# Kernel tuning notes

Measured on AMD Instinct MI355X. Metric: run time of the kernel, lower is better.

The kernel has to match this reference:

```python
import jax, jax.numpy as jnp
import numpy as np

THRESHOLD = 0.01
TOPK_RATIO = 0.7

def setup_inputs() -> dict:
    key = jax.random.key(0)
    k1, k2, k3, k4, k5 = jax.random.split(key, 5)
    B, N, F, K = 8, 2048, 512, 256
    x = jax.random.normal(k1, (B, N, F), dtype=jnp.float32)
    adj = jax.random.uniform(k2, (B, N, N), dtype=jnp.float32)
    mask = jnp.ones((B, N), dtype=jnp.float32)
    # assign_main = Linear(F->K), ReLU, Linear(K->K)
    W1 = jax.random.normal(k3, (F, K), dtype=jnp.float32) / np.sqrt(F)
    b1 = jnp.zeros((K,), dtype=jnp.float32)
    W2 = jax.random.normal(k4, (K, K), dtype=jnp.float32) / np.sqrt(K)
    b2 = jnp.zeros((K,), dtype=jnp.float32)
    return {"x": x, "adj": adj, "mask": mask, "W1": W1, "b1": b1, "W2": W2, "b2": b2}

def reference(x, adj, mask, W1, b1, W2, b2):
    B, N, Fdim = x.shape
    K = W2.shape[1]
    # soft assignment logits with masked softmax over clusters
    h = jax.nn.relu(jnp.einsum('bnf,fk->bnk', x, W1) + b1)
    logits = jnp.einsum('bnk,kl->bnl', h, W2) + b2            # [B,N,K]
    logits = logits + (-1e9) * (1.0 - mask[..., None])
    S = jax.nn.softmax(logits, axis=-1)                       # [B,N,K]
    # pooled features and pooled adjacency
    pfeat = jnp.einsum('bnk,bnf->bkf', S, x)                  # S^T x -> [B,K,F]
    mid = jnp.einsum('bnm,bmk->bnk', adj, S)                  # adj @ S
    pooled = jnp.einsum('bnk,bnl->bkl', S, mid)               # S^T adj S -> [B,K,K]
    # threshold + top-k sparsify with straight-through estimator
    topk = min(K, int(np.ceil(TOPK_RATIO * K)))
    thr_mask = (pooled >= THRESHOLD).astype(pooled.dtype)
    a_thr = pooled * thr_mask
    _, idx = jax.lax.top_k(a_thr, topk)                       # [B,K,topk]
    bi = jnp.arange(B)[:, None, None]
    ri = jnp.arange(K)[None, :, None]
    fmask = jnp.zeros_like(pooled).at[bi, ri, idx].set(1.0)
    a_sp = pooled * fmask
    a_ste = a_sp + jax.lax.stop_gradient(pooled - a_sp)       # forward == pooled
    # symmetric degree renormalization
    row_sum = a_ste.sum(axis=-1)
    d_inv_sqrt = 1.0 / jnp.sqrt(row_sum + 1e-9)
    pooled_adj = a_ste * d_inv_sqrt[:, :, None] * d_inv_sqrt[:, None, :]
    pmask = jnp.ones((B, K), dtype=x.dtype)
    return pfeat, pooled_adj, pmask
```

## Files before the change

### kernel.cpp

```cpp
#include <hip/hip_runtime.h>
#include <hip/hip_bf16.h>


typedef float f32x4 __attribute__((ext_vector_type(4)));
typedef __bf16 bf16x8 __attribute__((ext_vector_type(8)));

#define VMCNT(n) asm volatile("s_waitcnt vmcnt(" #n ")" ::: "memory")
#define LGKM0    asm volatile("s_waitcnt lgkmcnt(0)" ::: "memory")
#define SCHEDB   __builtin_amdgcn_sched_barrier(0)
#define BARRIER                                        \
  do {                                                 \
    LGKM0;                                             \
    __builtin_amdgcn_s_barrier();                      \
    asm volatile("" ::: "memory");                     \
    SCHEDB;                                            \
  } while (0)

__device__ __forceinline__ void async_load16(const void* g, void* l) {
  __builtin_amdgcn_global_load_lds((const __attribute__((address_space(1))) void*)g,
                                   (__attribute__((address_space(3))) void*)l, 16, 0, 0);
}
__device__ __forceinline__ unsigned short f2bf(float f) {
  return __builtin_bit_cast(unsigned short, (__bf16)f);
}
__device__ __forceinline__ ushort4 f4_to_bf4(float4 v) {
  ushort4 u; u.x = f2bf(v.x); u.y = f2bf(v.y); u.z = f2bf(v.z); u.w = f2bf(v.w); return u;
}

template <int ROWS, int BK, int NT>
__device__ __forceinline__ void stage_bf16(const __bf16* __restrict__ src, long long ld,
                                           __bf16* lds, int t) {
  constexpr int GR = BK / 8;
  constexpr int N = ROWS * GR / NT;
  static_assert(N >= 1, "stage too small");
#pragma unroll
  for (int c = 0; c < N; ++c) {
    const int idx = c * NT + t;
    const int row = idx / GR;
    const int g = idx % GR;
    const int gs = g ^ (row & (GR - 1) & 7);
    async_load16(src + (long long)row * ld + gs * 8, lds + idx * 8);
  }
}
template <int BK>
__device__ __forceinline__ bf16x8 frag(const __bf16* lds, int row, int kq) {
  constexpr int GR = BK / 8;
  const int g = kq ^ (row & (GR - 1) & 7);
  return *(const bf16x8*)(lds + row * BK + g * 8);
}

__global__ __launch_bounds__(256) void prep_k(const float* __restrict__ x,
                                              const float* __restrict__ W1,
                                              const float* __restrict__ W2,
                                              __bf16* __restrict__ xbT,
                                              __bf16* __restrict__ W1T,
                                              __bf16* __restrict__ W2T) {
  __shared__ float tile[64][65];
  const int tr = threadIdx.x >> 6, tc = threadIdx.x & 63;
  const int bid = blockIdx.x;
  const float* in; __bf16* out; int r0, c0, C, R;
  if (bid < 2048) {
    const int fb = bid >> 8, rest = bid & 255;
    const int nb = rest >> 3, b = rest & 7;
    in = x + (long long)b * 1048576; out = xbT + (long long)b * 1048576;
    r0 = nb * 64; c0 = fb * 64; R = 2048; C = 512;
  } else if (bid < 2080) {
    const int w = bid - 2048;
    in = W1; out = W1T; r0 = (w >> 2) * 64; c0 = (w & 3) * 64; R = 512; C = 256;
  } else {
    const int w = bid - 2080;
    in = W2; out = W2T; r0 = (w >> 2) * 64; c0 = (w & 3) * 64; R = 256; C = 256;
  }
#pragma unroll
  for (int i = 0; i < 16; ++i)
    tile[tr + i * 4][tc] = in[(long long)(r0 + tr + i * 4) * C + c0 + tc];
  __syncthreads();
#pragma unroll
  for (int i = 0; i < 16; ++i)
    out[(long long)(c0 + tr + i * 4) * R + r0 + tc] = (__bf16)tile[tc][tr + i * 4];
}

__device__ __forceinline__ void asg_compute(const __bf16* __restrict__ Abuf,
                                            const __bf16* __restrict__ Bbuf,
                                            f32x4 (&acc)[2][4], int wn, int l15, int l4) {
  bf16x8 af[2], bf[4];
#pragma unroll
  for (int i = 0; i < 2; ++i) af[i] = frag<32>(Abuf, i * 16 + l15, l4);
#pragma unroll
  for (int j = 0; j < 4; ++j) bf[j] = frag<32>(Bbuf, wn + j * 16 + l15, l4);
  __builtin_amdgcn_s_setprio(1);
#pragma unroll
  for (int i = 0; i < 2; ++i)
#pragma unroll
    for (int j = 0; j < 4; ++j)
      acc[i][j] = __builtin_amdgcn_mfma_f32_16x16x32_bf16(af[i], bf[j], acc[i][j], 0, 0, 0);
  __builtin_amdgcn_s_setprio(0);
}

__global__ __launch_bounds__(256) void assign_fused_k(
    const float* __restrict__ x, const __bf16* __restrict__ W1T,
    const __bf16* __restrict__ W2T, const float* __restrict__ b1,
    const float* __restrict__ b2, const float* __restrict__ mask,
    __bf16* __restrict__ ST) {
  __shared__ alignas(16) __bf16 Ax[2][32 * 32];
  __shared__ alignas(16) __bf16 Bw[2][256 * 32];
  __shared__ alignas(16) __bf16 hl[32 * 264];
  __shared__ float red[2][4][32];

  const int t = threadIdx.x;
  const int lane = t & 63, wave = t >> 6;
  const int l15 = lane & 15, l4 = lane >> 4;
  const int wn = wave * 64;
  const long long row0 = (long long)blockIdx.x * 32;
  const float* Xb = x + row0 * 512;

  const int arow = t >> 3, afq = t & 7;
  const int ag = afq >> 1;
  const int aoff = arow * 32 + ((ag ^ (arow & 3)) * 8) + (afq & 1) * 4;

  auto ldx = [&](int tile) -> float4 {
    return *(const float4*)(Xb + (long long)arow * 512 + tile * 32 + afq * 4);
  };
  auto sta = [&](__bf16* dst, float4 v) { *(ushort4*)&dst[aoff] = f4_to_bf4(v); };

  f32x4 acc[2][4] = {};

  float4 xA = ldx(0);
  SCHEDB;
  stage_bf16<256, 32, 256>(W1T, 512, Bw[0], t);
  SCHEDB;
  VMCNT(4); SCHEDB;
  sta(Ax[0], xA);
  float4 xB = ldx(1);
  SCHEDB;
  VMCNT(1); SCHEDB;
  BARRIER;

#pragma unroll 1
  for (int tt = 0; tt < 14; tt += 2) {
    stage_bf16<256, 32, 256>(W1T + (tt + 1) * 32, 512, Bw[1], t);
    SCHEDB;
    xA = ldx(tt + 2);
    SCHEDB;
    asg_compute(Ax[0], Bw[0], acc, wn, l15, l4);
    VMCNT(5); SCHEDB;
    sta(Ax[1], xB);
    VMCNT(1); SCHEDB;
    BARRIER;
    stage_bf16<256, 32, 256>(W1T + (tt + 2) * 32, 512, Bw[0], t);
    SCHEDB;
    xB = ldx(tt + 3);
    SCHEDB;
    asg_compute(Ax[1], Bw[1], acc, wn, l15, l4);
    VMCNT(5); SCHEDB;
    sta(Ax[0], xA);
    VMCNT(1); SCHEDB;
    BARRIER;
  }
  stage_bf16<256, 32, 256>(W1T + 15 * 32, 512, Bw[1], t);
  SCHEDB;
  asg_compute(Ax[0], Bw[0], acc, wn, l15, l4);
  VMCNT(4); SCHEDB;
  sta(Ax[1], xB);
  VMCNT(0); SCHEDB;
  BARRIER;
  asg_compute(Ax[1], Bw[1], acc, wn, l15, l4);

  stage_bf16<256, 32, 256>(W2T, 256, Bw[0], t);
  SCHEDB;
#pragma unroll
  for (int j = 0; j < 4; ++j) {
    const int col = wn + j * 16 + l15;
    const float bv = b1[col];
#pragma unroll
    for (int i = 0; i < 2; ++i)
#pragma unroll
      for (int r = 0; r < 4; ++r)
        hl[(i * 16 + l4 * 4 + r) * 264 + col] = (__bf16)fmaxf(acc[i][j][r] + bv, 0.f);
  }
  VMCNT(0); SCHEDB;
  BARRIER;

  f32x4 acc2[2][4] = {};
#pragma unroll 1
  for (int tt = 0; tt < 8; ++tt) {
    if (tt < 7) stage_bf16<256, 32, 256>(W2T + (tt + 1) * 32, 256, Bw[(tt & 1) ^ 1], t);
    SCHEDB;
    const __bf16* Bc = Bw[tt & 1];
    bf16x8 af[2], bf[4];
#pragma unroll
    for (int i = 0; i < 2; ++i)
      af[i] = *(const bf16x8*)(&hl[(i * 16 + l15) * 264 + tt * 32 + l4 * 8]);
#pragma unroll
    for (int j = 0; j < 4; ++j) bf[j] = frag<32>(Bc, wn + j * 16 + l15, l4);
#pragma unroll
    for (int i = 0; i < 2; ++i)
#pragma unroll
      for (int j = 0; j < 4; ++j)
        acc2[i][j] = __builtin_amdgcn_mfma_f32_16x16x32_bf16(af[i], bf[j], acc2[i][j], 0, 0, 0);
    VMCNT(0); SCHEDB;
    BARRIER;
  }

  float mb[2][4], mx[2][4], sm[2][4];
#pragma unroll
  for (int i = 0; i < 2; ++i)
#pragma unroll
    for (int r = 0; r < 4; ++r) {
      mb[i][r] = -1e9f * (1.0f - mask[row0 + i * 16 + l4 * 4 + r]);
      mx[i][r] = -3.4e38f;
      sm[i][r] = 0.f;
    }
#pragma unroll
  for (int j = 0; j < 4; ++j) {
    const float bv = b2[wn + j * 16 + l15];
#pragma unroll
    for (int i = 0; i < 2; ++i)
#pragma unroll
      for (int r = 0; r < 4; ++r) {
        const float v = acc2[i][j][r] + bv + mb[i][r];
        acc2[i][j][r] = v;
        mx[i][r] = fmaxf(mx[i][r], v);
      }
  }
#pragma unroll
  for (int i = 0; i < 2; ++i)
#pragma unroll
    for (int r = 0; r < 4; ++r) {
      float m = mx[i][r];
      m = fmaxf(m, __shfl_xor(m, 1, 64)); m = fmaxf(m, __shfl_xor(m, 2, 64));
      m = fmaxf(m, __shfl_xor(m, 4, 64)); m = fmaxf(m, __shfl_xor(m, 8, 64));
      mx[i][r] = m;
    }
  if (l15 == 0)
#pragma unroll
    for (int i = 0; i < 2; ++i)
#pragma unroll
      for (int r = 0; r < 4; ++r) red[0][wave][i * 16 + l4 * 4 + r] = mx[i][r];
  __syncthreads();
#pragma unroll
  for (int i = 0; i < 2; ++i)
#pragma unroll
    for (int r = 0; r < 4; ++r) {
      const int rl = i * 16 + l4 * 4 + r;
      mx[i][r] = fmaxf(fmaxf(red[0][0][rl], red[0][1][rl]),
                       fmaxf(red[0][2][rl], red[0][3][rl]));
    }
#pragma unroll
  for (int j = 0; j < 4; ++j)
#pragma unroll
    for (int i = 0; i < 2; ++i)
#pragma unroll
      for (int r = 0; r < 4; ++r) {
        const float e = __expf(acc2[i][j][r] - mx[i][r]);
        acc2[i][j][r] = e;
        sm[i][r] += e;
      }
#pragma unroll
  for (int i = 0; i < 2; ++i)
#pragma unroll
    for (int r = 0; r < 4; ++r) {
      float s = sm[i][r];
      s += __shfl_xor(s, 1, 64); s += __shfl_xor(s, 2, 64);
      s += __shfl_xor(s, 4, 64); s += __shfl_xor(s, 8, 64);
      sm[i][r] = s;
    }
  if (l15 == 0)
#pragma unroll
    for (int i = 0; i < 2; ++i)
#pragma unroll
      for (int r = 0; r < 4; ++r) red[1][wave][i * 16 + l4 * 4 + r] = sm[i][r];
  __syncthreads();
  float inv[2][4];
#pragma unroll
  for (int i = 0; i < 2; ++i)
#pragma unroll
    for (int r = 0; r < 4; ++r) {
      const int rl = i * 16 + l4 * 4 + r;
      inv[i][r] = 1.0f / (red[1][0][rl] + red[1][1][rl] + red[1][2][rl] + red[1][3][rl]);
    }
  const long long bb = row0 >> 11;
  const long long n0 = row0 & 2047;
  __bf16* Sb = ST + bb * 524288;
#pragma unroll
  for (int j = 0; j < 4; ++j) {
    const int col = wn + j * 16 + l15;
#pragma unroll
    for (int i = 0; i < 2; ++i) {
      ushort4 u;
      u.x = f2bf(acc2[i][j][0] * inv[i][0]);
      u.y = f2bf(acc2[i][j][1] * inv[i][1]);
      u.z = f2bf(acc2[i][j][2] * inv[i][2]);
      u.w = f2bf(acc2[i][j][3] * inv[i][3]);
      *(ushort4*)(Sb + (long long)col * 2048 + n0 + i * 16 + l4 * 4) = u;
    }
  }
}

__device__ __forceinline__ void adj_cmp(const __bf16* __restrict__ Abuf,
                                        const bf16x8* __restrict__ bq,
                                        f32x4 (&acc)[2][4], int l15, int l4) {
#pragma unroll
  for (int ks = 0; ks < 2; ++ks) {
    bf16x8 af[2];
#pragma unroll
    for (int i = 0; i < 2; ++i) af[i] = frag<64>(Abuf, i * 16 + l15, ks * 4 + l4);
    __builtin_amdgcn_s_setprio(1);
#pragma unroll
    for (int i = 0; i < 2; ++i)
#pragma unroll
      for (int j = 0; j < 4; ++j)
        acc[i][j] =
            __builtin_amdgcn_mfma_f32_16x16x32_bf16(af[i], bq[j * 2 + ks], acc[i][j], 0, 0, 0);
    __builtin_amdgcn_s_setprio(0);
  }
}

__global__ __launch_bounds__(256) void gemm_adj_k(const float* __restrict__ adj,
                                                  const __bf16* __restrict__ ST,
                                                  __bf16* __restrict__ midT) {
  __shared__ alignas(16) __bf16 Aa[2][32 * 64];
  const int t = threadIdx.x;
  const int lane = t & 63, wave = t >> 6;
  const int l15 = lane & 15, l4 = lane >> 4;
  const int wn = wave * 64;
  const int id = blockIdx.x;
  const int bz = id & 7;
  const long long r0 = (long long)(id >> 3) * 32;
  const float* Ab = adj + (long long)bz * 4194304 + r0 * 2048;
  const __bf16* Bb = ST + (long long)bz * 524288;

  const int arow = t >> 4, afq = t & 15;
  const int ag = afq >> 1;
  const int aoff0 = arow * 64 + ((ag ^ (arow & 7)) * 8) + (afq & 1) * 4;
  const int aoff1 = (arow + 16) * 64 + ((ag ^ ((arow + 16) & 7)) * 8) + (afq & 1) * 4;

  auto lda4 = [&](int tile, int half) -> float4 {
    return *(const float4*)(Ab + (long long)(arow + half * 16) * 2048 + tile * 64 + afq * 4);
  };
  auto sta = [&](__bf16* dst, float4 v0, float4 v1) {
    *(ushort4*)&dst[aoff0] = f4_to_bf4(v0);
    *(ushort4*)&dst[aoff1] = f4_to_bf4(v1);
  };
  auto ldb = [&](bf16x8* dst, int tile) {
#pragma unroll
    for (int j = 0; j < 4; ++j)
#pragma unroll
      for (int ks = 0; ks < 2; ++ks)
        dst[j * 2 + ks] = *(const bf16x8*)(Bb + (long long)(wn + j * 16 + l15) * 2048 +
                                           tile * 64 + ks * 32 + l4 * 8);
  };

  f32x4 acc[2][4] = {};
  bf16x8 b0[8], b1[8];

  float4 aA0 = lda4(0, 0), aA1 = lda4(0, 1);
  SCHEDB;
  ldb(b0, 0);
  SCHEDB;
  float4 aB0 = lda4(1, 0), aB1 = lda4(1, 1);
  SCHEDB;
  VMCNT(10); SCHEDB;
  sta(Aa[0], aA0, aA1);
  BARRIER;
  VMCNT(2); SCHEDB;

#pragma unroll 1
  for (int tt = 0; tt < 30; tt += 2) {
    ldb(b1, tt + 1);
    SCHEDB;
    aA0 = lda4(tt + 2, 0); aA1 = lda4(tt + 2, 1);
    SCHEDB;
    adj_cmp(Aa[0], b0, acc, l15, l4);
    VMCNT(10); SCHEDB;
    sta(Aa[1], aB0, aB1);
    BARRIER;
    VMCNT(2); SCHEDB;
    ldb(b0, tt + 2);
    SCHEDB;
    aB0 = lda4(tt + 3, 0); aB1 = lda4(tt + 3, 1);
    SCHEDB;
    adj_cmp(Aa[1], b1, acc, l15, l4);
    VMCNT(10); SCHEDB;
    sta(Aa[0], aA0, aA1);
    BARRIER;
    VMCNT(2); SCHEDB;
  }
  ldb(b1, 31);
  SCHEDB;
  adj_cmp(Aa[0], b0, acc, l15, l4);
  VMCNT(8); SCHEDB;
  sta(Aa[1], aB0, aB1);
  BARRIER;
  VMCNT(0); SCHEDB;
  adj_cmp(Aa[1], b1, acc, l15, l4);

  __bf16* Cb = midT + (long long)bz * 524288;
#pragma unroll
  for (int j = 0; j < 4; ++j) {
    const int l = wn + j * 16 + l15;
#pragma unroll
    for (int i = 0; i < 2; ++i) {
      ushort4 u;
      u.x = f2bf(acc[i][j][0]); u.y = f2bf(acc[i][j][1]);
      u.z = f2bf(acc[i][j][2]); u.w = f2bf(acc[i][j][3]);
      *(ushort4*)(Cb + (long long)l * 2048 + r0 + i * 16 + l4 * 4) = u;
    }
  }
}

__global__ __launch_bounds__(256) void gemm_feat_k(const __bf16* __restrict__ ST,
                                                   const __bf16* __restrict__ xbT,
                                                   float* __restrict__ pfeat) {
  __shared__ alignas(16) __bf16 As[3][32 * 64];
  __shared__ alignas(16) __bf16 Bs[3][64 * 64];
  const int t = threadIdx.x;
  const int lane = t & 63, wave = t >> 6;
  const int l15 = lane & 15, l4 = lane >> 4;
  const int wn = wave * 16;
  const int id = blockIdx.x;
  const int b = id & 7, j7 = id >> 3;
  const int kblk = j7 & 7, fblk = j7 >> 3;
  const __bf16* Ab = ST + (long long)b * 524288 + (long long)kblk * 32 * 2048;
  const __bf16* Bb = xbT + (long long)b * 1048576 + (long long)fblk * 64 * 2048;

  auto stage = [&](int s, int buf) {
    stage_bf16<32, 64, 256>(Ab + s * 64, 2048, (__bf16*)As + buf * 2048, t);
    stage_bf16<64, 64, 256>(Bb + s * 64, 2048, (__bf16*)Bs + buf * 4096, t);
  };
  auto cmp = [&](int buf, f32x4 (&acc)[2]) {
    const __bf16* Ac = (const __bf16*)As + buf * 2048;
    const __bf16* Bc = (const __bf16*)Bs + buf * 4096;
#pragma unroll
    for (int ks = 0; ks < 2; ++ks) {
      bf16x8 af[2], bf;
#pragma unroll
      for (int i = 0; i < 2; ++i) af[i] = frag<64>(Ac, i * 16 + l15, ks * 4 + l4);
      bf = frag<64>(Bc, wn + l15, ks * 4 + l4);
#pragma unroll
      for (int i = 0; i < 2; ++i)
        acc[i] = __builtin_amdgcn_mfma_f32_16x16x32_bf16(af[i], bf, acc[i], 0, 0, 0);
    }
  };

  f32x4 acc[2] = {};
  stage(0, 0);
  SCHEDB;
  stage(1, 1);
  SCHEDB;
  VMCNT(3); SCHEDB;
  BARRIER;

  int cur = 0, stg = 2;
#pragma unroll 1
  for (int tt = 0; tt < 30; ++tt) {
    stage(tt + 2, stg);
    SCHEDB;
    cmp(cur, acc);
    VMCNT(3); SCHEDB;
    BARRIER;
    cur = (cur == 2) ? 0 : cur + 1;
    stg = (stg == 2) ? 0 : stg + 1;
  }
  cmp(cur, acc);
  VMCNT(0); SCHEDB;
  BARRIER;
  cur = (cur == 2) ? 0 : cur + 1;
  cmp(cur, acc);

  float* out = pfeat + (long long)b * 131072;
#pragma unroll
  for (int i = 0; i < 2; ++i)
#pragma unroll
    for (int r = 0; r < 4; ++r)
      out[(long long)(kblk * 32 + i * 16 + l4 * 4 + r) * 512 + fblk * 64 + wn + l15] =
          acc[i][r];
}

__global__ __launch_bounds__(256) void gemm_pool_k(const __bf16* __restrict__ ST,
                                                   const __bf16* __restrict__ midT,
                                                   float* __restrict__ pooled) {
  __shared__ alignas(16) __bf16 As[3][32 * 64];
  __shared__ alignas(16) __bf16 Bs[3][32 * 64];
  const int t = threadIdx.x;
  const int lane = t & 63, wave = t >> 6;
  const int l15 = lane & 15, l4 = lane >> 4;
  const int wm = (wave >> 1) * 16, wn = (wave & 1) * 16;
  const int id = blockIdx.x;
  const int b = id & 7, j7 = id >> 3;
  const int kblk = j7 & 7, lblk = j7 >> 3;
  const __bf16* Ab = ST + (long long)b * 524288 + (long long)kblk * 32 * 2048;
  const __bf16* Bb = midT + (long long)b * 524288 + (long long)lblk * 32 * 2048;

  auto stage = [&](int s, int buf) {
    stage_bf16<32, 64, 256>(Ab + s * 64, 2048, (__bf16*)As + buf * 2048, t);
    stage_bf16<32, 64, 256>(Bb + s * 64, 2048, (__bf16*)Bs + buf * 2048, t);
  };
  auto cmp = [&](int buf, f32x4& acc) {
    const __bf16* Ac = (const __bf16*)As + buf * 2048;
    const __bf16* Bc = (const __bf16*)Bs + buf * 2048;
#pragma unroll
    for (int ks = 0; ks < 2; ++ks) {
      bf16x8 af = frag<64>(Ac, wm + l15, ks * 4 + l4);
      bf16x8 bf = frag<64>(Bc, wn + l15, ks * 4 + l4);
      acc = __builtin_amdgcn_mfma_f32_16x16x32_bf16(af, bf, acc, 0, 0, 0);
    }
  };

  f32x4 acc = {};
  stage(0, 0);
  SCHEDB;
  stage(1, 1);
  SCHEDB;
  VMCNT(2); SCHEDB;
  BARRIER;

  int cur = 0, stg = 2;
#pragma unroll 1
  for (int tt = 0; tt < 30; ++tt) {
    stage(tt + 2, stg);
    SCHEDB;
    cmp(cur, acc);
    VMCNT(2); SCHEDB;
    BARRIER;
    cur = (cur == 2) ? 0 : cur + 1;
    stg = (stg == 2) ? 0 : stg + 1;
  }
  cmp(cur, acc);
  VMCNT(0); SCHEDB;
  BARRIER;
  cur = (cur == 2) ? 0 : cur + 1;
  cmp(cur, acc);

  float* out = pooled + (long long)b * 65536;
#pragma unroll
  for (int r = 0; r < 4; ++r)
    out[(long long)(kblk * 32 + wm + l4 * 4 + r) * 256 + lblk * 32 + wn + l15] = acc[r];
}

__global__ __launch_bounds__(256) void rowsum_k(const float* __restrict__ pooled,
                                                float* __restrict__ dinv) {
  const int gr = blockIdx.x * 4 + (threadIdx.x >> 6);
  const int lane = threadIdx.x & 63;
  const float* p = pooled + (long long)gr * 256;
  float s = p[lane] + p[lane + 64] + p[lane + 128] + p[lane + 192];
#pragma unroll
  for (int o = 32; o > 0; o >>= 1) s += __shfl_xor(s, o, 64);
  if (lane == 0) dinv[gr] = rsqrtf(s + 1e-9f);
}

__global__ __launch_bounds__(256) void finalize_k(const float* __restrict__ pooled,
                                                  const float* __restrict__ dinv,
                                                  float* __restrict__ outAdj,
                                                  float* __restrict__ pmask) {
  const long long i = blockIdx.x * 256LL + threadIdx.x;
  const int c = (int)(i & 255);
  const int r = (int)((i >> 8) & 255);
  const int b = (int)(i >> 16);
  outAdj[i] = pooled[i] * dinv[b * 256 + r] * dinv[b * 256 + c];
  if (i < 2048) pmask[i] = 1.0f;
}

extern "C" void kernel_launch(void* const* d_in, const int* in_sizes, int n_in,
                              void* d_out, int out_size, void* d_ws, size_t ws_size,
                              hipStream_t stream) {
  (void)in_sizes; (void)n_in; (void)out_size; (void)ws_size;
  const float* x    = (const float*)d_in[0];
  const float* adj  = (const float*)d_in[1];
  const float* mask = (const float*)d_in[2];
  const float* W1   = (const float*)d_in[3];
  const float* b1   = (const float*)d_in[4];
  const float* W2   = (const float*)d_in[5];
  const float* b2   = (const float*)d_in[6];

  char* ws = (char*)d_ws;
  __bf16* ST     = (__bf16*)(ws + 0);
  __bf16* midT   = (__bf16*)(ws + 8388608);
  __bf16* xbT    = (__bf16*)(ws + 16777216);
  float*  pooled = (float*)(ws + 33554432);
  float*  dinv   = (float*)(ws + 35651584);
  __bf16* W1T    = (__bf16*)(ws + 35659776);
  __bf16* W2T    = (__bf16*)(ws + 35921920);

  float* pfeat  = (float*)d_out;
  float* outAdj = (float*)d_out + 1048576;
  float* pmask  = (float*)d_out + 1572864;

  prep_k<<<2096, 256, 0, stream>>>(x, W1, W2, xbT, W1T, W2T);
  assign_fused_k<<<512, 256, 0, stream>>>(x, W1T, W2T, b1, b2, mask, ST);
  gemm_feat_k<<<512, 256, 0, stream>>>(ST, xbT, pfeat);
  gemm_adj_k<<<512, 256, 0, stream>>>(adj, ST, midT);
  gemm_pool_k<<<512, 256, 0, stream>>>(ST, midT, pooled);
  rowsum_k<<<512, 256, 0, stream>>>(pooled, dinv);
  finalize_k<<<2048, 256, 0, stream>>>(pooled, dinv, outAdj, pmask);
}
```

Baseline: 139.8 us.

## Triple-buffer B fragments and deepen prefetch in adj@S GEMM loop

Restructures the adj @ S main loop into a 6-step unrolled pipeline that rotates three B register buffers, so B fragments are prefetched two tiles ahead instead of one. The hand-placed vmcnt waits and most sched barriers are removed, leaving the compiler to insert wait counts. The aim is to hide more global-load latency behind MFMA work. In exchange it uses more VGPRs, which can lower occupancy, and the compiler may insert more conservative waits than the manual schedule did.

```diff
diff --git a/kernel.cpp b/kernel.cpp
--- a/kernel.cpp
+++ b/kernel.cpp
@@ -335,14 +335,17 @@
   const int aoff0 = arow * 64 + ((ag ^ (arow & 7)) * 8) + (afq & 1) * 4;
   const int aoff1 = (arow + 16) * 64 + ((ag ^ ((arow + 16) & 7)) * 8) + (afq & 1) * 4;
 
-  auto lda4 = [&](int tile, int half) -> float4 {
-    return *(const float4*)(Ab + (long long)(arow + half * 16) * 2048 + tile * 64 + afq * 4);
+  auto lda0 = [&](int tile) -> float4 {
+    return *(const float4*)(Ab + (long long)arow * 2048 + tile * 64 + afq * 4);
+  };
+  auto lda1 = [&](int tile) -> float4 {
+    return *(const float4*)(Ab + (long long)(arow + 16) * 2048 + tile * 64 + afq * 4);
   };
   auto sta = [&](__bf16* dst, float4 v0, float4 v1) {
     *(ushort4*)&dst[aoff0] = f4_to_bf4(v0);
     *(ushort4*)&dst[aoff1] = f4_to_bf4(v1);
   };
-  auto ldb = [&](bf16x8* dst, int tile) {
+  auto ldb = [&](bf16x8(&dst)[8], int tile) {
 #pragma unroll
     for (int j = 0; j < 4; ++j)
 #pragma unroll
@@ -352,47 +355,41 @@
   };
 
   f32x4 acc[2][4] = {};
-  bf16x8 b0[8], b1[8];
-
-  float4 aA0 = lda4(0, 0), aA1 = lda4(0, 1);
-  SCHEDB;
+  bf16x8 b0[8], b1[8], b2[8];
+  float4 a0_0, a0_1, a1_0, a1_1;
+
+  a0_0 = lda0(0); a0_1 = lda1(0);
   ldb(b0, 0);
-  SCHEDB;
-  float4 aB0 = lda4(1, 0), aB1 = lda4(1, 1);
-  SCHEDB;
-  VMCNT(10); SCHEDB;
-  sta(Aa[0], aA0, aA1);
-  BARRIER;
-  VMCNT(2); SCHEDB;
+  a1_0 = lda0(1); a1_1 = lda1(1);
+  ldb(b1, 1);
+  SCHEDB;
+  sta(Aa[0], a0_0, a0_1);
+  BARRIER;
+
+  auto step = [&](int tile, bf16x8(&bIss)[8], bf16x8(&bUse)[8],
+                  float4& aI0, float4& aI1, float4& aS0, float4& aS1,
+                  const __bf16* Ard, __bf16* Awr) {
+    ldb(bIss, tile + 2);
+    aI0 = lda0(tile + 2); aI1 = lda1(tile + 2);
+    SCHEDB;
+    adj_cmp(Ard, bUse, acc, l15, l4);
+    sta(Awr, aS0, aS1);
+    BARRIER;
+  };
 
 #pragma unroll 1
-  for (int tt = 0; tt < 30; tt += 2) {
-    ldb(b1, tt + 1);
-    SCHEDB;
-    aA0 = lda4(tt + 2, 0); aA1 = lda4(tt + 2, 1);
-    SCHEDB;
-    adj_cmp(Aa[0], b0, acc, l15, l4);
-    VMCNT(10); SCHEDB;
-    sta(Aa[1], aB0, aB1);
-    BARRIER;
-    VMCNT(2); SCHEDB;
-    ldb(b0, tt + 2);
-    SCHEDB;
-    aB0 = lda4(tt + 3, 0); aB1 = lda4(tt + 3, 1);
-    SCHEDB;
-    adj_cmp(Aa[1], b1, acc, l15, l4);
-    VMCNT(10); SCHEDB;
-    sta(Aa[0], aA0, aA1);
-    BARRIER;
-    VMCNT(2); SCHEDB;
-  }
-  ldb(b1, 31);
-  SCHEDB;
+  for (int o = 0; o < 5; ++o) {
+    const int base = o * 6;
+    step(base + 0, b2, b0, a0_0, a0_1, a1_0, a1_1, Aa[0], Aa[1]);
+    step(base + 1, b0, b1, a1_0, a1_1, a0_0, a0_1, Aa[1], Aa[0]);
+    step(base + 2, b1, b2, a0_0, a0_1, a1_0, a1_1, Aa[0], Aa[1]);
+    step(base + 3, b2, b0, a1_0, a1_1, a0_0, a0_1, Aa[1], Aa[0]);
+    step(base + 4, b0, b1, a0_0, a0_1, a1_0, a1_1, Aa[0], Aa[1]);
+    step(base + 5, b1, b2, a1_0, a1_1, a0_0, a0_1, Aa[1], Aa[0]);
+  }
   adj_cmp(Aa[0], b0, acc, l15, l4);
-  VMCNT(8); SCHEDB;
-  sta(Aa[1], aB0, aB1);
-  BARRIER;
-  VMCNT(0); SCHEDB;
+  sta(Aa[1], a1_0, a1_1);
+  BARRIER;
   adj_cmp(Aa[1], b1, acc, l15, l4);
 
   __bf16* Cb = midT + (long long)bz * 524288;
```

Result: no change. 138.8 us (-0.7%).

## Merge independent kernels via block-role splitting and stage adjacency B operand through LDS

Applied to the files above, without the earlier changes.

Splits the prep kernel so weight transposes run alone, and folds the x transpose into the assignment kernel with one of every five blocks running the assignment and the rest transposing x. The adj@S and S^T x GEMMs are merged into one launch by alternating block roles. The adj GEMM now stages its S operand through LDS with async loads instead of holding it in registers. This removes two launches and lets independent work overlap. In exchange, the larger shared-memory footprint may lower occupancy, and the mixed block roles can imbalance the load.

```diff
diff --git a/kernel.cpp b/kernel.cpp
--- a/kernel.cpp
+++ b/kernel.cpp
@@ -49,28 +49,16 @@
   return *(const bf16x8*)(lds + row * BK + g * 8);
 }
 
-__global__ __launch_bounds__(256) void prep_k(const float* __restrict__ x,
-                                              const float* __restrict__ W1,
-                                              const float* __restrict__ W2,
-                                              __bf16* __restrict__ xbT,
-                                              __bf16* __restrict__ W1T,
-                                              __bf16* __restrict__ W2T) {
+__global__ __launch_bounds__(256) void prepW_k(const float* __restrict__ W1,
+                                               const float* __restrict__ W2,
+                                               __bf16* __restrict__ W1T,
+                                               __bf16* __restrict__ W2T) {
   __shared__ float tile[64][65];
   const int tr = threadIdx.x >> 6, tc = threadIdx.x & 63;
-  const int bid = blockIdx.x;
-  const float* in; __bf16* out; int r0, c0, C, R;
-  if (bid < 2048) {
-    const int fb = bid >> 8, rest = bid & 255;
-    const int nb = rest >> 3, b = rest & 7;
-    in = x + (long long)b * 1048576; out = xbT + (long long)b * 1048576;
-    r0 = nb * 64; c0 = fb * 64; R = 2048; C = 512;
-  } else if (bid < 2080) {
-    const int w = bid - 2048;
-    in = W1; out = W1T; r0 = (w >> 2) * 64; c0 = (w & 3) * 64; R = 512; C = 256;
-  } else {
-    const int w = bid - 2080;
-    in = W2; out = W2T; r0 = (w >> 2) * 64; c0 = (w & 3) * 64; R = 256; C = 256;
-  }
+  int w = blockIdx.x;
+  const float* in; __bf16* out; int r0, c0, R, C;
+  if (w < 32) { in = W1; out = W1T; r0 = (w >> 2) * 64; c0 = (w & 3) * 64; R = 512; C = 256; }
+  else { w -= 32; in = W2; out = W2T; r0 = (w >> 2) * 64; c0 = (w & 3) * 64; R = 256; C = 256; }
 #pragma unroll
   for (int i = 0; i < 16; ++i)
     tile[tr + i * 4][tc] = in[(long long)(r0 + tr + i * 4) * C + c0 + tc];
@@ -97,21 +85,46 @@
   __builtin_amdgcn_s_setprio(0);
 }
 
-__global__ __launch_bounds__(256) void assign_fused_k(
+__global__ __launch_bounds__(256) void k1_assign_prepx(
     const float* __restrict__ x, const __bf16* __restrict__ W1T,
     const __bf16* __restrict__ W2T, const float* __restrict__ b1,
     const float* __restrict__ b2, const float* __restrict__ mask,
-    __bf16* __restrict__ ST) {
-  __shared__ alignas(16) __bf16 Ax[2][32 * 32];
-  __shared__ alignas(16) __bf16 Bw[2][256 * 32];
-  __shared__ alignas(16) __bf16 hl[32 * 264];
-  __shared__ float red[2][4][32];
-
+    __bf16* __restrict__ ST, __bf16* __restrict__ xbT) {
+  __shared__ __align__(16) char smem[54784];
+  const int id = blockIdx.x;
   const int t = threadIdx.x;
+
+  if (id % 5 != 0) {
+    const int p = id - id / 5 - 1;
+    float* tile = (float*)smem;
+    const int tr = t >> 6, tc = t & 63;
+    const int fb = p >> 8, rest = p & 255;
+    const int nb = rest >> 3, b = rest & 7;
+    const float* in = x + (long long)b * 1048576;
+    __bf16* out = xbT + (long long)b * 1048576;
+    const int r0 = nb * 64, c0 = fb * 64;
+#pragma unroll
+    for (int i = 0; i < 16; ++i)
+      tile[(tr + i * 4) * 65 + tc] = in[(long long)(r0 + tr + i * 4) * 512 + c0 + tc];
+    __syncthreads();
+#pragma unroll
+    for (int i = 0; i < 16; ++i)
+      out[(long long)(c0 + tr + i * 4) * 2048 + r0 + tc] = (__bf16)tile[tc * 65 + tr + i * 4];
+    return;
+  }
+
+  const int a = id / 5;
+  __bf16* Ax0 = (__bf16*)smem;
+  __bf16* Ax1 = (__bf16*)(smem + 2048);
+  __bf16* Bw0 = (__bf16*)(smem + 4096);
+  __bf16* Bw1 = (__bf16*)(smem + 20480);
+  __bf16* hl  = (__bf16*)(smem + 36864);
+  float*  red = (float*)(smem + 53760);
+
   const int lane = t & 63, wave = t >> 6;
   const int l15 = lane & 15, l4 = lane >> 4;
   const int wn = wave * 64;
-  const long long row0 = (long long)blockIdx.x * 32;
+  const long long row0 = (long long)a * 32;
   const float* Xb = x + row0 * 512;
 
   const int arow = t >> 3, afq = t & 7;
@@ -127,10 +140,10 @@
 
   float4 xA = ldx(0);
   SCHEDB;
-  stage_bf16<256, 32, 256>(W1T, 512, Bw[0], t);
+  stage_bf16<256, 32, 256>(W1T, 512, Bw0, t);
   SCHEDB;
   VMCNT(4); SCHEDB;
-  sta(Ax[0], xA);
+  sta(Ax0, xA);
   float4 xB = ldx(1);
   SCHEDB;
   VMCNT(1); SCHEDB;
@@ -138,35 +151,35 @@
 
 #pragma unroll 1
   for (int tt = 0; tt < 14; tt += 2) {
-    stage_bf16<256, 32, 256>(W1T + (tt + 1) * 32, 512, Bw[1], t);
+    stage_bf16<256, 32, 256>(W1T + (tt + 1) * 32, 512, Bw1, t);
     SCHEDB;
     xA = ldx(tt + 2);
     SCHEDB;
-    asg_compute(Ax[0], Bw[0], acc, wn, l15, l4);
+    asg_compute(Ax0, Bw0, acc, wn, l15, l4);
     VMCNT(5); SCHEDB;
-    sta(Ax[1], xB);
+    sta(Ax1, xB);
     VMCNT(1); SCHEDB;
     BARRIER;
-    stage_bf16<256, 32, 256>(W1T + (tt + 2) * 32, 512, Bw[0], t);
+    stage_bf16<256, 32, 256>(W1T + (tt + 2) * 32, 512, Bw0, t);
     SCHEDB;
     xB = ldx(tt + 3);
     SCHEDB;
-    asg_compute(Ax[1], Bw[1], acc, wn, l15, l4);
+    asg_compute(Ax1, Bw1, acc, wn, l15, l4);
     VMCNT(5); SCHEDB;
-    sta(Ax[0], xA);
+    sta(Ax0, xA);
     VMCNT(1); SCHEDB;
     BARRIER;
   }
-  stage_bf16<256, 32, 256>(W1T + 15 * 32, 512, Bw[1], t);
-  SCHEDB;
-  asg_compute(Ax[0], Bw[0], acc, wn, l15, l4);
+  stage_bf16<256, 32, 256>(W1T + 15 * 32, 512, Bw1, t);
+  SCHEDB;
+  asg_compute(Ax0, Bw0, acc, wn, l15, l4);
   VMCNT(4); SCHEDB;
-  sta(Ax[1], xB);
+  sta(Ax1, xB);
   VMCNT(0); SCHEDB;
   BARRIER;
-  asg_compute(Ax[1], Bw[1], acc, wn, l15, l4);
-
-  stage_bf16<256, 32, 256>(W2T, 256, Bw[0], t);
+  asg_compute(Ax1, Bw1, acc, wn, l15, l4);
+
+  stage_bf16<256, 32, 256>(W2T, 256, Bw0, t);
   SCHEDB;
 #pragma unroll
   for (int j = 0; j < 4; ++j) {
@@ -184,9 +197,9 @@
   f32x4 acc2[2][4] = {};
 #pragma unroll 1
   for (int tt = 0; tt < 8; ++tt) {
-    if (tt < 7) stage_bf16<256, 32, 256>(W2T + (tt + 1) * 32, 256, Bw[(tt & 1) ^ 1], t);
-    SCHEDB;
-    const __bf16* Bc = Bw[tt & 1];
+    if (tt < 7) stage_bf16<256, 32, 256>(W2T + (tt + 1) * 32, 256, (tt & 1) ? Bw0 : Bw1, t);
+    SCHEDB;
+    const __bf16* Bc = (tt & 1) ? Bw1 : Bw0;
     bf16x8 af[2], bf[4];
 #pragma unroll
     for (int i = 0; i < 2; ++i)
@@ -236,15 +249,14 @@
 #pragma unroll
     for (int i = 0; i < 2; ++i)
 #pragma unroll
-      for (int r = 0; r < 4; ++r) red[0][wave][i * 16 + l4 * 4 + r] = mx[i][r];
+      for (int r = 0; r < 4; ++r) red[0 * 128 + wave * 32 + i * 16 + l4 * 4 + r] = mx[i][r];
   __syncthreads();
 #pragma unroll
   for (int i = 0; i < 2; ++i)
 #pragma unroll
     for (int r = 0; r < 4; ++r) {
       const int rl = i * 16 + l4 * 4 + r;
-      mx[i][r] = fmaxf(fmaxf(red[0][0][rl], red[0][1][rl]),
-                       fmaxf(red[0][2][rl], red[0][3][rl]));
+      mx[i][r] = fmaxf(fmaxf(red[rl], red[32 + rl]), fmaxf(red[64 + rl], red[96 + rl]));
     }
 #pragma unroll
   for (int j = 0; j < 4; ++j)
@@ -269,15 +281,15 @@
 #pragma unroll
     for (int i = 0; i < 2; ++i)
 #pragma unroll
-      for (int r = 0; r < 4; ++r) red[1][wave][i * 16 + l4 * 4 + r] = sm[i][r];
+      for (int r = 0; r < 4; ++r) red[128 + wave * 32 + i * 16 + l4 * 4 + r] = sm[i][r];
   __syncthreads();
   float inv[2][4];
 #pragma unroll
   for (int i = 0; i < 2; ++i)
 #pragma unroll
     for (int r = 0; r < 4; ++r) {
-      const int rl = i * 16 + l4 * 4 + r;
-      inv[i][r] = 1.0f / (red[1][0][rl] + red[1][1][rl] + red[1][2][rl] + red[1][3][rl]);
+      const int rl = 128 + i * 16 + l4 * 4 + r;
+      inv[i][r] = 1.0f / (red[rl] + red[rl + 32] + red[rl + 64] + red[rl + 96]);
     }
   const long long bb = row0 >> 11;
   const long long n0 = row0 & 2047;
@@ -297,140 +309,136 @@
   }
 }
 
-__device__ __forceinline__ void adj_cmp(const __bf16* __restrict__ Abuf,
-                                        const bf16x8* __restrict__ bq,
-                                        f32x4 (&acc)[2][4], int l15, int l4) {
+__device__ __forceinline__ void adj_compute(const __bf16* __restrict__ Abuf,
+                                            const __bf16* __restrict__ Bbuf,
+                                            f32x4 (&acc)[2][4],
+                                            int wn, int l15, int l4) {
 #pragma unroll
   for (int ks = 0; ks < 2; ++ks) {
-    bf16x8 af[2];
+    bf16x8 af[2], bf[4];
 #pragma unroll
     for (int i = 0; i < 2; ++i) af[i] = frag<64>(Abuf, i * 16 + l15, ks * 4 + l4);
+#pragma unroll
+    for (int j = 0; j < 4; ++j) bf[j] = frag<64>(Bbuf, wn + j * 16 + l15, ks * 4 + l4);
     __builtin_amdgcn_s_setprio(1);
 #pragma unroll
     for (int i = 0; i < 2; ++i)
 #pragma unroll
       for (int j = 0; j < 4; ++j)
-        acc[i][j] =
-            __builtin_amdgcn_mfma_f32_16x16x32_bf16(af[i], bq[j * 2 + ks], acc[i][j], 0, 0, 0);
+        acc[i][j] = __builtin_amdgcn_mfma_f32_16x16x32_bf16(af[i], bf[j], acc[i][j], 0, 0, 0);
     __builtin_amdgcn_s_setprio(0);
   }
 }
 
-__global__ __launch_bounds__(256) void gemm_adj_k(const float* __restrict__ adj,
-                                                  const __bf16* __restrict__ ST,
-                                                  __bf16* __restrict__ midT) {
-  __shared__ alignas(16) __bf16 Aa[2][32 * 64];
+__global__ __launch_bounds__(256) void k2_adj_feat(const float* __restrict__ adj,
+                                                   const __bf16* __restrict__ ST,
+                                                   __bf16* __restrict__ midT,
+                                                   const __bf16* __restrict__ xbT,
+                                                   float* __restrict__ pfeat) {
+  __shared__ __align__(16) char smem[73728];
   const int t = threadIdx.x;
   const int lane = t & 63, wave = t >> 6;
   const int l15 = lane & 15, l4 = lane >> 4;
-  const int wn = wave * 64;
-  const int id = blockIdx.x;
-  const int bz = id & 7;
-  const long long r0 = (long long)(id >> 3) * 32;
-  const float* Ab = adj + (long long)bz * 4194304 + r0 * 2048;
-  const __bf16* Bb = ST + (long long)bz * 524288;
-
-  const int arow = t >> 4, afq = t & 15;
-  const int ag = afq >> 1;
-  const int aoff0 = arow * 64 + ((ag ^ (arow & 7)) * 8) + (afq & 1) * 4;
-  const int aoff1 = (arow + 16) * 64 + ((ag ^ ((arow + 16) & 7)) * 8) + (afq & 1) * 4;
-
-  auto lda4 = [&](int tile, int half) -> float4 {
-    return *(const float4*)(Ab + (long long)(arow + half * 16) * 2048 + tile * 64 + afq * 4);
-  };
-  auto sta = [&](__bf16* dst, float4 v0, float4 v1) {
-    *(ushort4*)&dst[aoff0] = f4_to_bf4(v0);
-    *(ushort4*)&dst[aoff1] = f4_to_bf4(v1);
-  };
-  auto ldb = [&](bf16x8* dst, int tile) {
-#pragma unroll
-    for (int j = 0; j < 4; ++j)
-#pragma unroll
-      for (int ks = 0; ks < 2; ++ks)
-        dst[j * 2 + ks] = *(const bf16x8*)(Bb + (long long)(wn + j * 16 + l15) * 2048 +
-                                           tile * 64 + ks * 32 + l4 * 8);
-  };
-
-  f32x4 acc[2][4] = {};
-  bf16x8 b0[8], b1[8];
-
-  float4 aA0 = lda4(0, 0), aA1 = lda4(0, 1);
-  SCHEDB;
-  ldb(b0, 0);
-  SCHEDB;
-  float4 aB0 = lda4(1, 0), aB1 = lda4(1, 1);
-  SCHEDB;
-  VMCNT(10); SCHEDB;
-  sta(Aa[0], aA0, aA1);
-  BARRIER;
-  VMCNT(2); SCHEDB;
+
+  if ((blockIdx.x & 1) == 0) {
+    const int aid = blockIdx.x >> 1;
+    __bf16* Aa0 = (__bf16*)smem;
+    __bf16* Aa1 = (__bf16*)(smem + 4096);
+    __bf16* Bs0 = (__bf16*)(smem + 8192);
+    __bf16* Bs1 = (__bf16*)(smem + 40960);
+    const int wn = wave * 64;
+    const int bz = aid & 7;
+    const long long r0 = (long long)(aid >> 3) * 32;
+    const float* Ab = adj + (long long)bz * 4194304 + r0 * 2048;
+    const __bf16* Bb = ST + (long long)bz * 524288;
+
+    const int arow = t >> 4, afq = t & 15;
+    const int ag = afq >> 1;
+    const int aoff0 = arow * 64 + ((ag ^ (arow & 7)) * 8) + (afq & 1) * 4;
+    const int aoff1 = (arow + 16) * 64 + ((ag ^ ((arow + 16) & 7)) * 8) + (afq & 1) * 4;
+
+    auto lda4 = [&](int tile, int half) -> float4 {
+      return *(const float4*)(Ab + (long long)(arow + half * 16) * 2048 + tile * 64 + afq * 4);
+    };
+    auto sta = [&](__bf16* dst, float4 v0, float4 v1) {
+      *(ushort4*)&dst[aoff0] = f4_to_bf4(v0);
+      *(ushort4*)&dst[aoff1] = f4_to_bf4(v1);
+    };
+
+    f32x4 acc[2][4] = {};
+
+    float4 aA0 = lda4(0, 0), aA1 = lda4(0, 1);
+    SCHEDB;
+    stage_bf16<256, 64, 256>(Bb, 2048, Bs0, t);
+    SCHEDB;
+    VMCNT(8); SCHEDB;
+    sta(Aa0, aA0, aA1);
+    float4 aB0 = lda4(1, 0), aB1 = lda4(1, 1);
+    SCHEDB;
+    VMCNT(2); SCHEDB;
+    BARRIER;
 
 #pragma unroll 1
-  for (int tt = 0; tt < 30; tt += 2) {
-    ldb(b1, tt + 1);
-    SCHEDB;
-    aA0 = lda4(tt + 2, 0); aA1 = lda4(tt + 2, 1);
-    SCHEDB;
-    adj_cmp(Aa[0], b0, acc, l15, l4);
-    VMCNT(10); SCHEDB;
-    sta(Aa[1], aB0, aB1);
+    for (int tt = 0; tt < 30; tt += 2) {
+      stage_bf16<256, 64, 256>(Bb + (tt + 1) * 64, 2048, Bs1, t);
+      SCHEDB;
+      aA0 = lda4(tt + 2, 0); aA1 = lda4(tt + 2, 1);
+      SCHEDB;
+      adj_compute(Aa0, Bs0, acc, wn, l15, l4);
+      VMCNT(10); SCHEDB;
+      sta(Aa1, aB0, aB1);
+      VMCNT(2); SCHEDB;
+      BARRIER;
+      stage_bf16<256, 64, 256>(Bb + (tt + 2) * 64, 2048, Bs0, t);
+      SCHEDB;
+      aB0 = lda4(tt + 3, 0); aB1 = lda4(tt + 3, 1);
+      SCHEDB;
+      adj_compute(Aa1, Bs1, acc, wn, l15, l4);
+      VMCNT(10); SCHEDB;
+      sta(Aa0, aA0, aA1);
+      VMCNT(2); SCHEDB;
+      BARRIER;
+    }
+    stage_bf16<256, 64, 256>(Bb + 31 * 64, 2048, Bs1, t);
+    SCHEDB;
+    adj_compute(Aa0, Bs0, acc, wn, l15, l4);
+    VMCNT(8); SCHEDB;
+    sta(Aa1, aB0, aB1);
+    VMCNT(0); SCHEDB;
     BARRIER;
-    VMCNT(2); SCHEDB;
-    ldb(b0, tt + 2);
-    SCHEDB;
-    aB0 = lda4(tt + 3, 0); aB1 = lda4(tt + 3, 1);
-    SCHEDB;
-    adj_cmp(Aa[1], b1, acc, l15, l4);
-    VMCNT(10); SCHEDB;
-    sta(Aa[0], aA0, aA1);
-    BARRIER;
-    VMCNT(2); SCHEDB;
-  }
-  ldb(b1, 31);
-  SCHEDB;
-  adj_cmp(Aa[0], b0, acc, l15, l4);
-  VMCNT(8); SCHEDB;
-  sta(Aa[1], aB0, aB1);
-  BARRIER;
-  VMCNT(0); SCHEDB;
-  adj_cmp(Aa[1], b1, acc, l15, l4);
-
-  __bf16* Cb = midT + (long long)bz * 524288;
-#pragma unroll
-  for (int j = 0; j < 4; ++j) {
-    const int l = wn + j * 16 + l15;
-#pragma unroll
-    for (int i = 0; i < 2; ++i) {
-      ushort4 u;
-      u.x = f2bf(acc[i][j][0]); u.y = f2bf(acc[i][j][1]);
-      u.z = f2bf(acc[i][j][2]); u.w = f2bf(acc[i][j][3]);
-      *(ushort4*)(Cb + (long long)l * 2048 + r0 + i * 16 + l4 * 4) = u;
-    }
-  }
-}
-
-__global__ __launch_bounds__(256) void gemm_feat_k(const __bf16* __restrict__ ST,
-                                                   const __bf16* __restrict__ xbT,
-                                                   float* __restrict__ pfeat) {
-  __shared__ alignas(16) __bf16 As[3][32 * 64];
-  __shared__ alignas(16) __bf16 Bs[3][64 * 64];
-  const int t = threadIdx.x;
-  const int lane = t & 63, wave = t >> 6;
-  const int l15 = lane & 15, l4 = lane >> 4;
+    adj_compute(Aa1, Bs1, acc, wn, l15, l4);
+
+    __bf16* Cb = midT + (long long)bz * 524288;
+#pragma unroll
+    for (int j = 0; j < 4; ++j) {
+      const int l = wn + j * 16 + l15;
+#pragma unroll
+      for (int i = 0; i < 2; ++i) {
+        ushort4 u;
+        u.x = f2bf(acc[i][j][0]); u.y = f2bf(acc[i][j][1]);
+        u.z = f2bf(acc[i][j][2]); u.w = f2bf(acc[i][j][3]);
+        *(ushort4*)(Cb + (long long)l * 2048 + r0 + i * 16 + l4 * 4) = u;
+      }
+    }
+    return;
+  }
+
+  const int fid = blockIdx.x >> 1;
+  __bf16* AsB = (__bf16*)smem;
+  __bf16* BsB = (__bf16*)(smem + 12288);
   const int wn = wave * 16;
-  const int id = blockIdx.x;
-  const int b = id & 7, j7 = id >> 3;
+  const int b = fid & 7, j7 = fid >> 3;
   const int kblk = j7 & 7, fblk = j7 >> 3;
   const __bf16* Ab = ST + (long long)b * 524288 + (long long)kblk * 32 * 2048;
   const __bf16* Bb = xbT + (long long)b * 1048576 + (long long)fblk * 64 * 2048;
 
   auto stage = [&](int s, int buf) {
-    stage_bf16<32, 64, 256>(Ab + s * 64, 2048, (__bf16*)As + buf * 2048, t);
-    stage_bf16<64, 64, 256>(Bb + s * 64, 2048, (__bf16*)Bs + buf * 4096, t);
+    stage_bf16<32, 64, 256>(Ab + s * 64, 2048, AsB + buf * 2048, t);
+    stage_bf16<64, 64, 256>(Bb + s * 64, 2048, BsB + buf * 4096, t);
   };
   auto cmp = [&](int buf, f32x4 (&acc)[2]) {
-    const __bf16* Ac = (const __bf16*)As + buf * 2048;
-    const __bf16* Bc = (const __bf16*)Bs + buf * 4096;
+    const __bf16* Ac = AsB + buf * 2048;
+    const __bf16* Bc = BsB + buf * 4096;
 #pragma unroll
     for (int ks = 0; ks < 2; ++ks) {
       bf16x8 af[2], bf;
@@ -586,10 +594,9 @@
   float* outAdj = (float*)d_out + 1048576;
   float* pmask  = (float*)d_out + 1572864;
 
-  prep_k<<<2096, 256, 0, stream>>>(x, W1, W2, xbT, W1T, W2T);
-  assign_fused_k<<<512, 256, 0, stream>>>(x, W1T, W2T, b1, b2, mask, ST);
-  gemm_feat_k<<<512, 256, 0, stream>>>(ST, xbT, pfeat);
-  gemm_adj_k<<<512, 256, 0, stream>>>(adj, ST, midT);
+  prepW_k<<<48, 256, 0, stream>>>(W1, W2, W1T, W2T);
+  k1_assign_prepx<<<2560, 256, 0, stream>>>(x, W1T, W2T, b1, b2, mask, ST, xbT);
+  k2_adj_feat<<<1024, 256, 0, stream>>>(adj, ST, midT, xbT, pfeat);
   gemm_pool_k<<<512, 256, 0, stream>>>(ST, midT, pooled);
   rowsum_k<<<512, 256, 0, stream>>>(pooled, dinv);
   finalize_k<<<2048, 256, 0, stream>>>(pooled, dinv, outAdj, pmask);
```

Result: no change. 139.2 us (-0.4%).

## Retile adj GEMM to 64x128 blocks with LDS-staged S tiles

Applied to the files above, without the earlier changes.

Reshapes the adj@S kernel so each block computes a 64-row by 128-column output tile, with waves in a 2x2 grid, instead of 32 rows by all 256 columns. The S operand is now staged into a triple-buffered LDS tile through async loads, rather than each wave loading its own fragments straight from global memory into registers. This frees registers and shares S loads across waves. The cost is that each adj row tile is now read by two blocks (one per column half), more LDS traffic, and a changed block count and grid mapping.

```diff
diff --git a/kernel.cpp b/kernel.cpp
--- a/kernel.cpp
+++ b/kernel.cpp
@@ -297,114 +297,112 @@
   }
 }
 
-__device__ __forceinline__ void adj_cmp(const __bf16* __restrict__ Abuf,
-                                        const bf16x8* __restrict__ bq,
-                                        f32x4 (&acc)[2][4], int l15, int l4) {
-#pragma unroll
-  for (int ks = 0; ks < 2; ++ks) {
-    bf16x8 af[2];
-#pragma unroll
-    for (int i = 0; i < 2; ++i) af[i] = frag<64>(Abuf, i * 16 + l15, ks * 4 + l4);
-    __builtin_amdgcn_s_setprio(1);
-#pragma unroll
-    for (int i = 0; i < 2; ++i)
-#pragma unroll
-      for (int j = 0; j < 4; ++j)
-        acc[i][j] =
-            __builtin_amdgcn_mfma_f32_16x16x32_bf16(af[i], bq[j * 2 + ks], acc[i][j], 0, 0, 0);
-    __builtin_amdgcn_s_setprio(0);
-  }
-}
-
 __global__ __launch_bounds__(256) void gemm_adj_k(const float* __restrict__ adj,
                                                   const __bf16* __restrict__ ST,
                                                   __bf16* __restrict__ midT) {
-  __shared__ alignas(16) __bf16 Aa[2][32 * 64];
+  __shared__ alignas(16) __bf16 Aa[2][64 * 64];
+  __shared__ alignas(16) __bf16 Bs[3][128 * 64];
   const int t = threadIdx.x;
   const int lane = t & 63, wave = t >> 6;
   const int l15 = lane & 15, l4 = lane >> 4;
-  const int wn = wave * 64;
+  const int wr = (wave >> 1) * 32;
+  const int wc = (wave & 1) * 64;
   const int id = blockIdx.x;
   const int bz = id & 7;
-  const long long r0 = (long long)(id >> 3) * 32;
+  const int nh = (id >> 3) & 1;
+  const long long r0 = (long long)(id >> 4) * 64;
   const float* Ab = adj + (long long)bz * 4194304 + r0 * 2048;
-  const __bf16* Bb = ST + (long long)bz * 524288;
+  const __bf16* Bb = ST + (long long)bz * 524288 + (long long)nh * 128 * 2048;
 
   const int arow = t >> 4, afq = t & 15;
-  const int ag = afq >> 1;
-  const int aoff0 = arow * 64 + ((ag ^ (arow & 7)) * 8) + (afq & 1) * 4;
-  const int aoff1 = (arow + 16) * 64 + ((ag ^ ((arow + 16) & 7)) * 8) + (afq & 1) * 4;
-
-  auto lda4 = [&](int tile, int half) -> float4 {
-    return *(const float4*)(Ab + (long long)(arow + half * 16) * 2048 + tile * 64 + afq * 4);
-  };
-  auto sta = [&](__bf16* dst, float4 v0, float4 v1) {
-    *(ushort4*)&dst[aoff0] = f4_to_bf4(v0);
-    *(ushort4*)&dst[aoff1] = f4_to_bf4(v1);
-  };
-  auto ldb = [&](bf16x8* dst, int tile) {
-#pragma unroll
-    for (int j = 0; j < 4; ++j)
-#pragma unroll
-      for (int ks = 0; ks < 2; ++ks)
-        dst[j * 2 + ks] = *(const bf16x8*)(Bb + (long long)(wn + j * 16 + l15) * 2048 +
-                                           tile * 64 + ks * 32 + l4 * 8);
+  auto ldA = [&](int tile, float4 (&r)[4]) {
+#pragma unroll
+    for (int c = 0; c < 4; ++c)
+      r[c] = *(const float4*)(Ab + (long long)(arow + c * 16) * 2048 + tile * 64 + afq * 4);
+  };
+  auto stA = [&](__bf16* dst, const float4 (&r)[4]) {
+#pragma unroll
+    for (int c = 0; c < 4; ++c) {
+      const int row = arow + c * 16;
+      const int off = row * 64 + (((afq >> 1) ^ (row & 7)) * 8) + (afq & 1) * 4;
+      *(ushort4*)&dst[off] = f4_to_bf4(r[c]);
+    }
   };
 
   f32x4 acc[2][4] = {};
-  bf16x8 b0[8], b1[8];
-
-  float4 aA0 = lda4(0, 0), aA1 = lda4(0, 1);
-  SCHEDB;
-  ldb(b0, 0);
-  SCHEDB;
-  float4 aB0 = lda4(1, 0), aB1 = lda4(1, 1);
-  SCHEDB;
-  VMCNT(10); SCHEDB;
-  sta(Aa[0], aA0, aA1);
-  BARRIER;
-  VMCNT(2); SCHEDB;
-
+  float4 rA[4], rB[4];
+
+  auto cmp = [&](const __bf16* Ac, const __bf16* Bc) {
+#pragma unroll
+    for (int ks = 0; ks < 2; ++ks) {
+      bf16x8 af[2], bf[4];
+#pragma unroll
+      for (int i = 0; i < 2; ++i) af[i] = frag<64>(Ac, wr + i * 16 + l15, ks * 4 + l4);
+#pragma unroll
+      for (int j = 0; j < 4; ++j) bf[j] = frag<64>(Bc, wc + j * 16 + l15, ks * 4 + l4);
+      __builtin_amdgcn_s_setprio(1);
+#pragma unroll
+      for (int i = 0; i < 2; ++i)
+#pragma unroll
+        for (int j = 0; j < 4; ++j)
+          acc[i][j] = __builtin_amdgcn_mfma_f32_16x16x32_bf16(af[i], bf[j], acc[i][j], 0, 0, 0);
+      __builtin_amdgcn_s_setprio(0);
+    }
+  };
+
+  stage_bf16<128, 64, 256>(Bb, 2048, Bs[0], t);
+  SCHEDB;
+  ldA(0, rA);
+  SCHEDB;
+  stage_bf16<128, 64, 256>(Bb + 64, 2048, Bs[1], t);
+  SCHEDB;
+  ldA(1, rB);
+  SCHEDB;
+  VMCNT(8); SCHEDB;
+  stA(Aa[0], rA);
+  BARRIER;
+
+  int curB = 0, stgB = 2;
 #pragma unroll 1
   for (int tt = 0; tt < 30; tt += 2) {
-    ldb(b1, tt + 1);
-    SCHEDB;
-    aA0 = lda4(tt + 2, 0); aA1 = lda4(tt + 2, 1);
-    SCHEDB;
-    adj_cmp(Aa[0], b0, acc, l15, l4);
-    VMCNT(10); SCHEDB;
-    sta(Aa[1], aB0, aB1);
-    BARRIER;
-    VMCNT(2); SCHEDB;
-    ldb(b0, tt + 2);
-    SCHEDB;
-    aB0 = lda4(tt + 3, 0); aB1 = lda4(tt + 3, 1);
-    SCHEDB;
-    adj_cmp(Aa[1], b1, acc, l15, l4);
-    VMCNT(10); SCHEDB;
-    sta(Aa[0], aA0, aA1);
-    BARRIER;
-    VMCNT(2); SCHEDB;
-  }
-  ldb(b1, 31);
-  SCHEDB;
-  adj_cmp(Aa[0], b0, acc, l15, l4);
-  VMCNT(8); SCHEDB;
-  sta(Aa[1], aB0, aB1);
-  BARRIER;
+    stage_bf16<128, 64, 256>(Bb + (tt + 2) * 64, 2048, Bs[stgB], t);
+    SCHEDB;
+    ldA(tt + 2, rA);
+    SCHEDB;
+    cmp(Aa[0], Bs[curB]);
+    VMCNT(8); SCHEDB;
+    stA(Aa[1], rB);
+    BARRIER;
+    curB = (curB == 2) ? 0 : curB + 1;
+    stgB = (stgB == 2) ? 0 : stgB + 1;
+    stage_bf16<128, 64, 256>(Bb + (tt + 3) * 64, 2048, Bs[stgB], t);
+    SCHEDB;
+    ldA(tt + 3, rB);
+    SCHEDB;
+    cmp(Aa[1], Bs[curB]);
+    VMCNT(8); SCHEDB;
+    stA(Aa[0], rA);
+    BARRIER;
+    curB = (curB == 2) ? 0 : curB + 1;
+    stgB = (stgB == 2) ? 0 : stgB + 1;
+  }
+  cmp(Aa[0], Bs[curB]);
   VMCNT(0); SCHEDB;
-  adj_cmp(Aa[1], b1, acc, l15, l4);
+  stA(Aa[1], rB);
+  BARRIER;
+  curB = (curB == 2) ? 0 : curB + 1;
+  cmp(Aa[1], Bs[curB]);
 
   __bf16* Cb = midT + (long long)bz * 524288;
 #pragma unroll
   for (int j = 0; j < 4; ++j) {
-    const int l = wn + j * 16 + l15;
+    const int l = nh * 128 + wc + j * 16 + l15;
 #pragma unroll
     for (int i = 0; i < 2; ++i) {
       ushort4 u;
       u.x = f2bf(acc[i][j][0]); u.y = f2bf(acc[i][j][1]);
       u.z = f2bf(acc[i][j][2]); u.w = f2bf(acc[i][j][3]);
-      *(ushort4*)(Cb + (long long)l * 2048 + r0 + i * 16 + l4 * 4) = u;
+      *(ushort4*)(Cb + (long long)l * 2048 + r0 + wr + i * 16 + l4 * 4) = u;
     }
   }
 }
```

Result: faster. 113.5 us (-18.8%).
